# Kernel optimization log

Measured on AMD Instinct MI355X. Metric: run time of the kernel, lower is better.

## Reference

```python
import jax, jax.numpy as jnp
import numpy as np

B, CIN, HID, T, W, H, TAU = 8, 16, 64, 4, 32, 32, 5
EPS = 1e-5
DN = ('NCDHW', 'OIDHW', 'NCDHW')


def conv3d(x, w, b):
    # 'same' conv3d, NCDHW layout
    y = jax.lax.conv_general_dilated(x, w, (1, 1, 1), 'SAME', dimension_numbers=DN)
    return y + b[None, :, None, None, None]


def ln3(u):
    # F.layer_norm over the last 3 (spatial) dims, no affine
    mu = jnp.mean(u, axis=(-3, -2, -1), keepdims=True)
    var = jnp.var(u, axis=(-3, -2, -1), keepdims=True)
    return (u - mu) * jax.lax.rsqrt(var + EPS)


def ln4(u, w, b):
    # nn.LayerNorm(memory_shape): over last 4 dims (C,T,W,H), with affine
    mu = jnp.mean(u, axis=(-4, -3, -2, -1), keepdims=True)
    var = jnp.var(u, axis=(-4, -3, -2, -1), keepdims=True)
    return (u - mu) * jax.lax.rsqrt(var + EPS) * w + b


def self_attention(r, c_history):
    scale = 1.0 / np.sqrt(T * W * H)
    scores = jnp.einsum('bctwh,lbctwh->bl', r, c_history) * scale  # [B, TAU]
    # faithful to source: softmax over dim=0 (the batch axis of the [b,l] scores)
    attn = jax.nn.softmax(scores, axis=0)
    return jnp.einsum('bl,lbctwh->bctwh', attn, c_history)


def setup_inputs() -> dict:
    key = jax.random.key(0)
    ks = jax.random.split(key, 8)
    x = jax.random.normal(ks[0], (B, CIN, T, W, H), jnp.float32)
    c_history = jax.random.normal(ks[1], (TAU, B, HID, T, W, H), jnp.float32)
    m = jax.random.normal(ks[2], (B, HID, T, W, H), jnp.float32)
    h = jax.random.normal(ks[3], (B, HID, T, W, H), jnp.float32)
    Wx = jax.random.normal(ks[4], (7, HID, CIN, 3, 3, 3), jnp.float32) * 0.05
    bx = jnp.zeros((7, HID), jnp.float32)
    # 9 state-branch conv kernels: [hr, hi, hg, mi', mg', mf', ho, co, mo]
    Wh = jax.random.normal(ks[5], (9, HID, HID, 3, 3, 3), jnp.float32) * 0.02
    bh = jnp.zeros((9, HID), jnp.float32)
    w111 = jax.random.normal(ks[6], (HID, 2 * HID, 1, 1, 1), jnp.float32) * 0.05
    b111 = jnp.zeros((HID,), jnp.float32)
    ln_w = jnp.ones((HID, T, W, H), jnp.float32)
    ln_b = jnp.zeros((HID, T, W, H), jnp.float32)
    return dict(x=x, c_history=c_history, m=m, h=h, Wx=Wx, bx=bx, Wh=Wh, bh=bh,
                w111=w111, b111=b111, ln_w=ln_w, ln_b=ln_b)


def reference(x, c_history, m, h, Wx, bx, Wh, bh, w111, b111, ln_w, ln_b):
    cx = lambda i: conv3d(x, Wx[i], bx[i])
    cs = lambda u, i: conv3d(u, Wh[i], bh[i])
    r = jax.nn.sigmoid(ln3(cx(0) + cs(h, 0)))
    i = jax.nn.sigmoid(ln3(cx(1) + cs(h, 1)))
    g = jnp.tanh(ln3(cx(2) + cs(h, 2)))
    recall = self_attention(r, c_history)
    c = i * g + ln4(c_history[-1] + recall, ln_w, ln_b)
    i_p = jax.nn.sigmoid(ln3(cx(3) + cs(m, 3)))
    g_p = jnp.tanh(ln3(cx(4) + cs(m, 4)))
    f_p = jax.nn.sigmoid(ln3(cx(5) + cs(m, 5)))
    m_new = i_p * g_p + f_p * m
    o = jax.nn.sigmoid(ln3(cx(6) + cs(h, 6) + cs(c, 7) + cs(m_new, 8)))
    h_new = o * jnp.tanh(conv3d(jnp.concatenate([c, m_new], axis=1), w111, b111))
    c_history_new = jnp.concatenate([c_history[1:], c[None]], axis=0)
    return (c_history_new, m_new, h_new)
```

## Files before the change

kernel.cpp:

```cpp
#include <hip/hip_runtime.h>
#include <hip/hip_bf16.h>
#include <math.h>

#define BATCH 8
#define CIN 16
#define HID 64
#define S2 1024
#define SP 4096
#define CHB 262144
#define TAU 5
#define GATE_SZ 2097152
#define EPS 1e-5f

#define WS_Z_OFF   ((size_t)3 * GATE_SZ)
#define WS_ST_OFF  ((size_t)4 * GATE_SZ)

typedef unsigned short u16;
typedef __attribute__((ext_vector_type(8))) short  short8;
typedef __attribute__((ext_vector_type(8))) u16    ushort8;
typedef __attribute__((ext_vector_type(4))) float  f32x4;

#define N7 (7*27*64*96)
#define NO (27*64*128)
#define N1 (64*128)

__device__ __forceinline__ u16 f2b(float v) {
    __hip_bfloat16 h = __float2bfloat16(v);
    u16 r; __builtin_memcpy(&r, &h, 2); return r;
}

__device__ __forceinline__ float* gate_ptr(float* out, float* ws, int g) {
    return (g < 4) ? (out + (size_t)g * GATE_SZ) : (ws + (size_t)(g - 4) * GATE_SZ);
}

__global__ __launch_bounds__(256) void pack_w_k(const float* __restrict__ Wx,
                                                const float* __restrict__ Wh,
                                                const float* __restrict__ w111,
                                                u16* __restrict__ A7, u16* __restrict__ Ao,
                                                u16* __restrict__ A111)
{
    const int idx = blockIdx.x * 256 + threadIdx.x;
    if (idx < N7) {
        const int k = idx % 96, oc = (idx / 96) % 64, tap = (idx / (96*64)) % 27, g = idx / (96*64*27);
        float v = 0.f;
        if (k < 16)      v = Wx[((size_t)(g*64 + oc)*16 + k)      * 27 + tap];
        else if (k < 80) v = Wh[((size_t)(g*64 + oc)*64 + (k-16)) * 27 + tap];
        A7[idx] = f2b(v);
    } else if (idx < N7 + NO) {
        const int j = idx - N7;
        const int k = j % 128, oc = (j / 128) % 64, tap = j / (128*64);
        float v = (k < 64) ? Wh[((size_t)(7*64 + oc)*64 + k)      * 27 + tap]
                           : Wh[((size_t)(8*64 + oc)*64 + (k-64)) * 27 + tap];
        Ao[j] = f2b(v);
    } else if (idx < N7 + NO + N1) {
        const int j = idx - N7 - NO;
        A111[j] = f2b(w111[j]);
    }
}

__global__ __launch_bounds__(256) void pack_xhm_k(const float* __restrict__ x,
                                                  const float* __restrict__ h,
                                                  const float* __restrict__ m,
                                                  u16* __restrict__ XH, u16* __restrict__ XM)
{
    __shared__ float t[144][65];
    const int bi = blockIdx.x, b = bi >> 6, s0 = (bi & 63) << 6;
    for (int i = threadIdx.x; i < 144*64; i += 256) {
        const int row = i >> 6, sc = i & 63;
        float v;
        if (row < 16)      v = x[((size_t)b*16 + row)      * SP + s0 + sc];
        else if (row < 80) v = h[((size_t)b*64 + (row-16)) * SP + s0 + sc];
        else               v = m[((size_t)b*64 + (row-80)) * SP + s0 + sc];
        t[row][sc] = v;
    }
    __syncthreads();
    for (int j = threadIdx.x; j < 64*96; j += 256) {
        const int s = j / 96, ch = j % 96;
        const size_t o = ((size_t)b*4096 + s0 + s) * 96 + ch;
        XH[o] = f2b(ch < 80 ? t[ch][s] : 0.f);
        XM[o] = f2b(ch < 16 ? t[ch][s] : (ch < 80 ? t[ch + 64][s] : 0.f));
    }
}

template<int KCH, int TAPS, int NR, int MODE>
__global__ __launch_bounds__(256, 3) void conv_mfma_k(
    const u16* __restrict__ XA, const u16* __restrict__ XB,
    const u16* __restrict__ Apack,
    const float* __restrict__ bxp, const float* __restrict__ bhp,
    const float* __restrict__ b111,
    float* __restrict__ out, float* __restrict__ ws)
{
    constexpr int YT   = NR + 2;
    constexpr int ROWS = 4 * YT * 34;
    constexpr int PADK = 40;
    __shared__ __align__(16) u16 xs[ROWS * PADK];

    const int bi = blockIdx.x;
    int g = 0, b, y0, kh = 0, kc_lo = 0, kc_hi = KCH / 32;
    const u16* X; const u16* Ag; float* outp;
    if (MODE == 0) {
        constexpr int YB = 32 / NR;
        g  = bi / (8 * YB);
        b  = (bi / YB) % 8;
        y0 = (bi % YB) * NR;
        X  = (g >= 3 && g <= 5) ? XB : XA;
        Ag = Apack + (size_t)g * TAPS * 64 * KCH;
        outp = gate_ptr(out, ws, g) + (size_t)b * CHB;
    } else if (MODE == 1) {
        kh = bi >> 8; b = (bi >> 5) & 7; y0 = bi & 31;
        kc_lo = kh * 2; kc_hi = kc_lo + 2;
        X = XA; Ag = Apack;
        outp = ws + (size_t)2 * GATE_SZ + (size_t)b * CHB;
    } else {
        b = bi >> 5; y0 = bi & 31;
        X = XA; Ag = Apack;
        outp = ws + (size_t)b * CHB;
    }
    const u16* Xb = X + (size_t)b * 4096 * KCH;

    const int tid  = threadIdx.x;
    const int w    = tid >> 6;
    const int lane = tid & 63;
    const int xn   = lane & 15, quad = lane >> 4;

    f32x4 acc[4][2 * NR] = {};

    for (int kc = kc_lo; kc < kc_hi; ++kc) {
        if (kc != kc_lo) __syncthreads();
        for (int cix = tid; cix < ROWS * 4; cix += 256) {
            const int r = cix >> 2, sub = cix & 3;
            const int t = r / (YT * 34), rem = r % (YT * 34);
            const int yy = rem / 34, xx = rem % 34;
            const int gy = y0 + yy - 1, gx = xx - 1;
            ushort8 v = {0, 0, 0, 0, 0, 0, 0, 0};
            if ((unsigned)gy < 32u && (unsigned)gx < 32u)
                v = *(const ushort8*)&Xb[(size_t)(t * 1024 + gy * 32 + gx) * KCH + kc * 32 + sub * 8];
            *(ushort8*)&xs[r * PADK + sub * 8] = v;
        }
        __syncthreads();

        auto load_a = [&](short8* a, int tap) {
            #pragma unroll
            for (int mt = 0; mt < 4; ++mt)
                a[mt] = *(const short8*)&Ag[(size_t)(tap * 64 + mt * 16 + xn) * KCH + kc * 32 + quad * 8];
        };
        auto load_b = [&](short8* bf, int tap) {
            int kd, ky, kx;
            if (TAPS == 27) { kd = tap / 9; ky = (tap / 3) % 3; kx = tap % 3; }
            else            { kd = 1; ky = 1; kx = 1; }
            const int tin = w + kd - 1;
            #pragma unroll
            for (int nt = 0; nt < 2 * NR; ++nt) {
                const int ysub = nt >> 1, xh = nt & 1;
                bf[nt] = *(const short8*)
                    &xs[((tin * YT + ysub + ky) * 34 + xh * 16 + xn + kx) * PADK + quad * 8];
            }
        };
        auto do_mfma = [&](short8* a, short8* bf) {
            #pragma unroll
            for (int nt = 0; nt < 2 * NR; ++nt)
                #pragma unroll
                for (int mt = 0; mt < 4; ++mt)
                    acc[mt][nt] = __builtin_amdgcn_mfma_f32_16x16x32_bf16(a[mt], bf[nt], acc[mt][nt], 0, 0, 0);
        };

        if (TAPS == 27) {
            const int tap_lo = (w == 0) ? 9 : 0;
            const int tap_hi = (w == 3) ? 18 : 27;
            short8 a0[4], b0[2 * NR], a1[4], b1[2 * NR];
            load_a(a0, tap_lo); load_b(b0, tap_lo);
            int tap = tap_lo;
            for (; tap + 2 <= tap_hi; tap += 2) {
                load_a(a1, tap + 1); load_b(b1, tap + 1);
                do_mfma(a0, b0);
                if (tap + 2 < tap_hi) { load_a(a0, tap + 2); load_b(b0, tap + 2); }
                do_mfma(a1, b1);
            }
            if (tap < tap_hi) do_mfma(a0, b0);
        } else {
            short8 a0[4], b0[2 * NR];
            load_a(a0, 0); load_b(b0, 0);
            do_mfma(a0, b0);
        }
    }

    #pragma unroll
    for (int mt = 0; mt < 4; ++mt)
    #pragma unroll
    for (int nt = 0; nt < 2 * NR; ++nt) {
        const int ysub = nt >> 1, xh = nt & 1;
        const int sp = w * 1024 + (y0 + ysub) * 32 + xh * 16 + xn;
        #pragma unroll
        for (int reg = 0; reg < 4; ++reg) {
            const int oc = mt * 16 + quad * 4 + reg;
            float bias;
            if (MODE == 0)      bias = bxp[g * 64 + oc] + bhp[g * 64 + oc];
            else if (MODE == 1) bias = (kh == 0) ? (bhp[7 * 64 + oc] + bhp[8 * 64 + oc]) : 0.f;
            else                bias = b111[oc];
            const float vv = acc[mt][nt][reg] + bias;
            float* p = outp + (size_t)oc * SP + sp;
            if (MODE == 1) atomicAdd(p, vv); else *p = vv;
        }
    }
}

__global__ __launch_bounds__(256) void ln3_act_k(float* __restrict__ out,
                                                 float* __restrict__ ws, int gate0)
{
    const int blk = blockIdx.x;
    const int g = gate0 + (blk >> 9);
    float* p = gate_ptr(out, ws, g) + (size_t)(blk & 511) * SP;
    const int tid = threadIdx.x;

    float s = 0.f, s2 = 0.f;
    for (int k = tid; k < SP; k += 256) { float v = p[k]; s += v; s2 += v * v; }
    #pragma unroll
    for (int off = 32; off > 0; off >>= 1) { s += __shfl_down(s, off); s2 += __shfl_down(s2, off); }
    __shared__ float rs[4], rs2[4], stat[2];
    if ((tid & 63) == 0) { rs[tid >> 6] = s; rs2[tid >> 6] = s2; }
    __syncthreads();
    if (tid == 0) {
        float S  = rs[0] + rs[1] + rs[2] + rs[3];
        float Sq = rs2[0] + rs2[1] + rs2[2] + rs2[3];
        float mu  = S * (1.f / SP);
        float var = Sq * (1.f / SP) - mu * mu;
        stat[0] = mu; stat[1] = rsqrtf(var + EPS);
    }
    __syncthreads();
    const float mu = stat[0], r = stat[1];
    const bool use_tanh = (g == 2 || g == 4);
    for (int k = tid; k < SP; k += 256) {
        float v = (p[k] - mu) * r;
        p[k] = use_tanh ? tanhf(v) : 1.f / (1.f + expf(-v));
    }
}

__global__ __launch_bounds__(256) void scores_k(const float* __restrict__ r,
                                                const float* __restrict__ chist,
                                                float* __restrict__ stats)
{
    const int blk = blockIdx.x;
    const int chunk = blk & 7;
    const int bl = blk >> 3;
    const int l = bl % 5, b = bl / 5;
    const float* rp = r + (size_t)b * CHB;
    const float* cp = chist + (size_t)(l * BATCH + b) * CHB;
    float s = 0.f;
    const int lo = chunk * (CHB / 8);
    for (int k = lo + threadIdx.x; k < lo + CHB / 8; k += 256) s += rp[k] * cp[k];
    #pragma unroll
    for (int off = 32; off > 0; off >>= 1) s += __shfl_down(s, off);
    __shared__ float rsh[4];
    if ((threadIdx.x & 63) == 0) rsh[threadIdx.x >> 6] = s;
    __syncthreads();
    if (threadIdx.x == 0)
        atomicAdd(&stats[l * 8 + b], (rsh[0] + rsh[1] + rsh[2] + rsh[3]) * (1.f / 64.f));
}

__global__ void softmax_k(float* __restrict__ stats)
{
    int l = threadIdx.x;
    if (l < TAU) {
        float mx = -1e30f;
        for (int b = 0; b < BATCH; ++b) mx = fmaxf(mx, stats[l * 8 + b]);
        float e[BATCH]; float sum = 0.f;
        for (int b = 0; b < BATCH; ++b) { e[b] = expf(stats[l * 8 + b] - mx); sum += e[b]; }
        for (int b = 0; b < BATCH; ++b) stats[40 + l * 8 + b] = e[b] / sum;
    }
}

__global__ __launch_bounds__(256) void recall_k(const float* __restrict__ chist,
                                                float* __restrict__ ws,
                                                float* __restrict__ part)
{
    const float* stats = ws + WS_ST_OFF;
    const int blk = blockIdx.x;
    const int b = blk >> 10;
    const int idx = (blk & 1023) * 256 + threadIdx.x;
    const float a0 = stats[40 +  0 + b], a1 = stats[40 +  8 + b], a2 = stats[40 + 16 + b];
    const float a3 = stats[40 + 24 + b], a4 = stats[40 + 32 + b];
    const size_t e = (size_t)b * CHB + idx;
    const size_t LB = (size_t)BATCH * CHB;
    float z = chist[4 * LB + e] * (1.f + a4)
            + a0 * chist[0 * LB + e] + a1 * chist[1 * LB + e]
            + a2 * chist[2 * LB + e] + a3 * chist[3 * LB + e];
    ws[WS_Z_OFF + e] = z;

    float s = z, s2 = z * z;
    #pragma unroll
    for (int off = 32; off > 0; off >>= 1) { s += __shfl_down(s, off); s2 += __shfl_down(s2, off); }
    __shared__ float rs[4], rs2[4];
    if ((threadIdx.x & 63) == 0) { rs[threadIdx.x >> 6] = s; rs2[threadIdx.x >> 6] = s2; }
    __syncthreads();
    if (threadIdx.x == 0) {
        part[blk]        = rs[0] + rs[1] + rs[2] + rs[3];
        part[8192 + blk] = rs2[0] + rs2[1] + rs2[2] + rs2[3];
    }
}

__global__ __launch_bounds__(256) void ln4_stats_k(const float* __restrict__ part,
                                                   float* __restrict__ stats)
{
    const int b = blockIdx.x;
    float s = 0.f, s2 = 0.f;
    for (int j = threadIdx.x; j < 1024; j += 256) {
        s  += part[b * 1024 + j];
        s2 += part[8192 + b * 1024 + j];
    }
    #pragma unroll
    for (int off = 32; off > 0; off >>= 1) { s += __shfl_down(s, off); s2 += __shfl_down(s2, off); }
    __shared__ float rs[4], rs2[4];
    if ((threadIdx.x & 63) == 0) { rs[threadIdx.x >> 6] = s; rs2[threadIdx.x >> 6] = s2; }
    __syncthreads();
    if (threadIdx.x == 0) {
        float S  = rs[0] + rs[1] + rs[2] + rs[3];
        float Sq = rs2[0] + rs2[1] + rs2[2] + rs2[3];
        float mu  = S * (1.f / CHB);
        float var = Sq * (1.f / CHB) - mu * mu;
        stats[80 + b] = mu;
        stats[88 + b] = rsqrtf(var + EPS);
    }
}

__global__ __launch_bounds__(256) void cm_pcm_k(float* __restrict__ out, float* __restrict__ ws,
                                                const float* __restrict__ m,
                                                const float* __restrict__ lnw,
                                                const float* __restrict__ lnb,
                                                u16* __restrict__ PCM)
{
    __shared__ __align__(16) u16 tl[64][136];
    const int bi = blockIdx.x;
    const int b = bi >> 6;
    const int s0 = (bi & 63) << 6;
    const float* stats = ws + WS_ST_OFF;
    const float mu = stats[80 + b], rstd = stats[88 + b];

    for (int i = threadIdx.x; i < 1024; i += 256) {
        const int chn = i >> 4;
        const int sp4 = (i & 15) << 2;
        const size_t e = (size_t)b * CHB + (size_t)chn * SP + s0 + sp4;
        const size_t le = (size_t)chn * SP + s0 + sp4;
        float4 z  = *(const float4*)&ws[WS_Z_OFF + e];
        float4 gi = *(const float4*)&gate_ptr(out, ws, 1)[e];
        float4 gg = *(const float4*)&gate_ptr(out, ws, 2)[e];
        float4 ip = *(const float4*)&gate_ptr(out, ws, 3)[e];
        float4 gp = *(const float4*)&gate_ptr(out, ws, 4)[e];
        float4 fp = *(const float4*)&gate_ptr(out, ws, 5)[e];
        float4 mm = *(const float4*)&m[e];
        float4 lw = *(const float4*)&lnw[le];
        float4 lb = *(const float4*)&lnb[le];
        float4 c, mn;
        c.x = gi.x * gg.x + (z.x - mu) * rstd * lw.x + lb.x;
        c.y = gi.y * gg.y + (z.y - mu) * rstd * lw.y + lb.y;
        c.z = gi.z * gg.z + (z.z - mu) * rstd * lw.z + lb.z;
        c.w = gi.w * gg.w + (z.w - mu) * rstd * lw.w + lb.w;
        mn.x = ip.x * gp.x + fp.x * mm.x;
        mn.y = ip.y * gp.y + fp.y * mm.y;
        mn.z = ip.z * gp.z + fp.z * mm.z;
        mn.w = ip.w * gp.w + fp.w * mm.w;
        *(float4*)&out[(size_t)4 * GATE_SZ + e] = c;
        *(float4*)&out[(size_t)5 * GATE_SZ + e] = mn;
        const float cc[4] = {c.x, c.y, c.z, c.w};
        const float mm2[4] = {mn.x, mn.y, mn.z, mn.w};
        #pragma unroll
        for (int k = 0; k < 4; ++k) {
            tl[sp4 + k][chn]      = f2b(cc[k]);
            tl[sp4 + k][64 + chn] = f2b(mm2[k]);
        }
    }
    __syncthreads();
    for (int j = threadIdx.x; j < 1024; j += 256) {
        const int s = j >> 4, c8 = (j & 15) << 3;
        ushort8 v = *(const ushort8*)&tl[s][c8];
        *(ushort8*)&PCM[((size_t)b * 4096 + s0 + s) * 128 + c8] = v;
    }
}

__global__ __launch_bounds__(256) void hnew_elem_k(const float* __restrict__ o,
                                                   const float* __restrict__ v,
                                                   float* __restrict__ hn)
{
    const size_t i = (size_t)blockIdx.x * 256 + threadIdx.x;
    float4 ov = ((const float4*)o)[i], vv = ((const float4*)v)[i];
    float4 r;
    r.x = ov.x * tanhf(vv.x); r.y = ov.y * tanhf(vv.y);
    r.z = ov.z * tanhf(vv.z); r.w = ov.w * tanhf(vv.w);
    ((float4*)hn)[i] = r;
}

__global__ __launch_bounds__(256) void hist_copy_k(const float* __restrict__ chist,
                                                   float* __restrict__ out)
{
    const size_t i = (size_t)blockIdx.x * 256 + threadIdx.x;
    const float4* src = (const float4*)(chist + GATE_SZ);
    float4* dst = (float4*)out;
    dst[i] = src[i];
}

extern "C" void kernel_launch(void* const* d_in, const int* in_sizes, int n_in,
                              void* d_out, int out_size, void* d_ws, size_t ws_size,
                              hipStream_t stream)
{
    const float* x    = (const float*)d_in[0];
    const float* ch   = (const float*)d_in[1];
    const float* m    = (const float*)d_in[2];
    const float* h    = (const float*)d_in[3];
    const float* Wx   = (const float*)d_in[4];
    const float* bx   = (const float*)d_in[5];
    const float* Wh   = (const float*)d_in[6];
    const float* bh   = (const float*)d_in[7];
    const float* w111 = (const float*)d_in[8];
    const float* b111 = (const float*)d_in[9];
    const float* lnw  = (const float*)d_in[10];
    const float* lnb  = (const float*)d_in[11];
    float* out = (float*)d_out;
    float* ws  = (float*)d_ws;

    u16* XH   = (u16*)(out + (size_t)4 * GATE_SZ);
    u16* A7   = (u16*)(out + (size_t)5 * GATE_SZ);
    u16* XM   = (u16*)(out + (size_t)6 * GATE_SZ);
    u16* Ao   = XM + (size_t)BATCH * 4096 * 96;
    u16* A111 = Ao + (size_t)NO;
    u16* PCM  = (u16*)out;
    float* part  = out + (size_t)4 * GATE_SZ;
    float* stats = ws + WS_ST_OFF;

    hipMemsetAsync(stats, 0, 128 * sizeof(float), stream);
    pack_w_k<<<(N7 + NO + N1 + 255) / 256, 256, 0, stream>>>(Wx, Wh, w111, A7, Ao, A111);
    pack_xhm_k<<<512, 256, 0, stream>>>(x, h, m, XH, XM);

    conv_mfma_k<96, 27, 2, 0><<<896, 256, 0, stream>>>(XH, XM, A7, bx, bh, nullptr, out, ws);
    ln3_act_k<<<3072, 256, 0, stream>>>(out, ws, 0);

    scores_k<<<BATCH * TAU * 8, 256, 0, stream>>>(out, ch, stats);
    softmax_k<<<1, 64, 0, stream>>>(stats);
    recall_k<<<8192, 256, 0, stream>>>(ch, ws, part);
    ln4_stats_k<<<8, 256, 0, stream>>>(part, stats);
    cm_pcm_k<<<512, 256, 0, stream>>>(out, ws, m, lnw, lnb, PCM);

    conv_mfma_k<128, 27, 1, 1><<<512, 256, 0, stream>>>(PCM, nullptr, Ao, nullptr, bh, nullptr, out, ws);
    ln3_act_k<<<512, 256, 0, stream>>>(out, ws, 6);
    conv_mfma_k<128, 1, 1, 2><<<256, 256, 0, stream>>>(PCM, nullptr, A111, nullptr, nullptr, b111, out, ws);

    hnew_elem_k<<<GATE_SZ / 1024, 256, 0, stream>>>(ws + (size_t)2 * GATE_SZ, ws, out + (size_t)6 * GATE_SZ);
    hist_copy_k<<<8192, 256, 0, stream>>>(ch, out);
}
```

Before: 438.5 us.

## Swizzle conv LDS tile, raise occupancy, and fuse small attention/LN4/tail kernels

The conv kernel's shared-memory input tile drops its padding in favour of an XOR swizzle, which shrinks LDS use, and the occupancy hint goes from 3 to 4 blocks per CU. The scores kernel now reads r once per element for all five history steps. The softmax is folded into recall_k, the LN4 statistics into cm_pcm_k, the stats memset into pack_w_k, and hnew plus the history copy into one tail kernel. These changes cut launch count and repeated loads, at the cost of redundant per-block softmax and LN4-stat computation and possible register pressure at the higher occupancy target.

```diff
diff --git a/kernel.cpp b/kernel.cpp
--- a/kernel.cpp
+++ b/kernel.cpp
@@ -37,8 +37,10 @@
                                                 const float* __restrict__ Wh,
                                                 const float* __restrict__ w111,
                                                 u16* __restrict__ A7, u16* __restrict__ Ao,
-                                                u16* __restrict__ A111)
-{
+                                                u16* __restrict__ A111,
+                                                float* __restrict__ stats)
+{
+    if (blockIdx.x == 0 && threadIdx.x < 128) stats[threadIdx.x] = 0.f;
     const int idx = blockIdx.x * 256 + threadIdx.x;
     if (idx < N7) {
         const int k = idx % 96, oc = (idx / 96) % 64, tap = (idx / (96*64)) % 27, g = idx / (96*64*27);
@@ -82,8 +84,12 @@
     }
 }
 
+__device__ __forceinline__ int swz32(int r, int c) {
+    return r * 32 + ((c ^ ((r >> 1) & 3)) << 3);
+}
+
 template<int KCH, int TAPS, int NR, int MODE>
-__global__ __launch_bounds__(256, 3) void conv_mfma_k(
+__global__ __launch_bounds__(256, 4) void conv_mfma_k(
     const u16* __restrict__ XA, const u16* __restrict__ XB,
     const u16* __restrict__ Apack,
     const float* __restrict__ bxp, const float* __restrict__ bhp,
@@ -92,7 +98,7 @@
 {
     constexpr int YT   = NR + 2;
     constexpr int ROWS = 4 * YT * 34;
-    constexpr int PADK = 40;
+    constexpr int PADK = 32;
     __shared__ __align__(16) u16 xs[ROWS * PADK];
 
     const int bi = blockIdx.x;
@@ -135,7 +141,7 @@
             ushort8 v = {0, 0, 0, 0, 0, 0, 0, 0};
             if ((unsigned)gy < 32u && (unsigned)gx < 32u)
                 v = *(const ushort8*)&Xb[(size_t)(t * 1024 + gy * 32 + gx) * KCH + kc * 32 + sub * 8];
-            *(ushort8*)&xs[r * PADK + sub * 8] = v;
+            *(ushort8*)&xs[swz32(r, sub)] = v;
         }
         __syncthreads();
 
@@ -152,8 +158,8 @@
             #pragma unroll
             for (int nt = 0; nt < 2 * NR; ++nt) {
                 const int ysub = nt >> 1, xh = nt & 1;
-                bf[nt] = *(const short8*)
-                    &xs[((tin * YT + ysub + ky) * 34 + xh * 16 + xn + kx) * PADK + quad * 8];
+                const int row = (tin * YT + ysub + ky) * 34 + xh * 16 + xn + kx;
+                bf[nt] = *(const short8*)&xs[swz32(row, quad)];
             }
         };
         auto do_mfma = [&](short8* a, short8* bf) {
@@ -240,32 +246,28 @@
                                                 float* __restrict__ stats)
 {
     const int blk = blockIdx.x;
-    const int chunk = blk & 7;
-    const int bl = blk >> 3;
-    const int l = bl % 5, b = bl / 5;
+    const int b = blk >> 6, chunk = blk & 63;
     const float* rp = r + (size_t)b * CHB;
-    const float* cp = chist + (size_t)(l * BATCH + b) * CHB;
-    float s = 0.f;
-    const int lo = chunk * (CHB / 8);
-    for (int k = lo + threadIdx.x; k < lo + CHB / 8; k += 256) s += rp[k] * cp[k];
-    #pragma unroll
-    for (int off = 32; off > 0; off >>= 1) s += __shfl_down(s, off);
-    __shared__ float rsh[4];
-    if ((threadIdx.x & 63) == 0) rsh[threadIdx.x >> 6] = s;
-    __syncthreads();
-    if (threadIdx.x == 0)
-        atomicAdd(&stats[l * 8 + b], (rsh[0] + rsh[1] + rsh[2] + rsh[3]) * (1.f / 64.f));
-}
-
-__global__ void softmax_k(float* __restrict__ stats)
-{
-    int l = threadIdx.x;
-    if (l < TAU) {
-        float mx = -1e30f;
-        for (int b = 0; b < BATCH; ++b) mx = fmaxf(mx, stats[l * 8 + b]);
-        float e[BATCH]; float sum = 0.f;
-        for (int b = 0; b < BATCH; ++b) { e[b] = expf(stats[l * 8 + b] - mx); sum += e[b]; }
-        for (int b = 0; b < BATCH; ++b) stats[40 + l * 8 + b] = e[b] / sum;
+    const int lo = chunk * (CHB / 64);
+    float s[TAU] = {};
+    for (int k = lo + threadIdx.x; k < lo + CHB / 64; k += 256) {
+        const float rv = rp[k];
+        #pragma unroll
+        for (int l = 0; l < TAU; ++l) s[l] += rv * chist[(size_t)(l * BATCH + b) * CHB + k];
+    }
+    __shared__ float rsh[TAU][4];
+    #pragma unroll
+    for (int l = 0; l < TAU; ++l) {
+        float v = s[l];
+        #pragma unroll
+        for (int off = 32; off > 0; off >>= 1) v += __shfl_down(v, off);
+        if ((threadIdx.x & 63) == 0) rsh[l][threadIdx.x >> 6] = v;
+    }
+    __syncthreads();
+    if (threadIdx.x < TAU) {
+        const int l = threadIdx.x;
+        atomicAdd(&stats[l * 8 + b],
+                  (rsh[l][0] + rsh[l][1] + rsh[l][2] + rsh[l][3]) * (1.f / 64.f));
     }
 }
 
@@ -277,8 +279,23 @@
     const int blk = blockIdx.x;
     const int b = blk >> 10;
     const int idx = (blk & 1023) * 256 + threadIdx.x;
-    const float a0 = stats[40 +  0 + b], a1 = stats[40 +  8 + b], a2 = stats[40 + 16 + b];
-    const float a3 = stats[40 + 24 + b], a4 = stats[40 + 32 + b];
+
+    __shared__ float attn[TAU];
+    if (threadIdx.x < TAU) {
+        const int l = threadIdx.x;
+        float mx = -1e30f;
+        for (int bb = 0; bb < BATCH; ++bb) mx = fmaxf(mx, stats[l * 8 + bb]);
+        float sum = 0.f, e = 0.f;
+        for (int bb = 0; bb < BATCH; ++bb) {
+            float t = expf(stats[l * 8 + bb] - mx);
+            sum += t;
+            if (bb == b) e = t;
+        }
+        attn[l] = e / sum;
+    }
+    __syncthreads();
+    const float a0 = attn[0], a1 = attn[1], a2 = attn[2], a3 = attn[3], a4 = attn[4];
+
     const size_t e = (size_t)b * CHB + idx;
     const size_t LB = (size_t)BATCH * CHB;
     float z = chist[4 * LB + e] * (1.f + a4)
@@ -298,10 +315,18 @@
     }
 }
 
-__global__ __launch_bounds__(256) void ln4_stats_k(const float* __restrict__ part,
-                                                   float* __restrict__ stats)
-{
-    const int b = blockIdx.x;
+__global__ __launch_bounds__(256) void cm_pcm_k(float* __restrict__ out, float* __restrict__ ws,
+                                                const float* __restrict__ m,
+                                                const float* __restrict__ lnw,
+                                                const float* __restrict__ lnb,
+                                                const float* __restrict__ part,
+                                                u16* __restrict__ PCM)
+{
+    __shared__ __align__(16) u16 tl[64][136];
+    const int bi = blockIdx.x;
+    const int b = bi >> 6;
+    const int s0 = (bi & 63) << 6;
+
     float s = 0.f, s2 = 0.f;
     for (int j = threadIdx.x; j < 1024; j += 256) {
         s  += part[b * 1024 + j];
@@ -309,7 +334,7 @@
     }
     #pragma unroll
     for (int off = 32; off > 0; off >>= 1) { s += __shfl_down(s, off); s2 += __shfl_down(s2, off); }
-    __shared__ float rs[4], rs2[4];
+    __shared__ float rs[4], rs2[4], st[2];
     if ((threadIdx.x & 63) == 0) { rs[threadIdx.x >> 6] = s; rs2[threadIdx.x >> 6] = s2; }
     __syncthreads();
     if (threadIdx.x == 0) {
@@ -317,23 +342,10 @@
         float Sq = rs2[0] + rs2[1] + rs2[2] + rs2[3];
         float mu  = S * (1.f / CHB);
         float var = Sq * (1.f / CHB) - mu * mu;
-        stats[80 + b] = mu;
-        stats[88 + b] = rsqrtf(var + EPS);
-    }
-}
-
-__global__ __launch_bounds__(256) void cm_pcm_k(float* __restrict__ out, float* __restrict__ ws,
-                                                const float* __restrict__ m,
-                                                const float* __restrict__ lnw,
-                                                const float* __restrict__ lnb,
-                                                u16* __restrict__ PCM)
-{
-    __shared__ __align__(16) u16 tl[64][136];
-    const int bi = blockIdx.x;
-    const int b = bi >> 6;
-    const int s0 = (bi & 63) << 6;
-    const float* stats = ws + WS_ST_OFF;
-    const float mu = stats[80 + b], rstd = stats[88 + b];
+        st[0] = mu; st[1] = rsqrtf(var + EPS);
+    }
+    __syncthreads();
+    const float mu = st[0], rstd = st[1];
 
     for (int i = threadIdx.x; i < 1024; i += 256) {
         const int chn = i >> 4;
@@ -370,31 +382,29 @@
     }
     __syncthreads();
     for (int j = threadIdx.x; j < 1024; j += 256) {
-        const int s = j >> 4, c8 = (j & 15) << 3;
-        ushort8 v = *(const ushort8*)&tl[s][c8];
-        *(ushort8*)&PCM[((size_t)b * 4096 + s0 + s) * 128 + c8] = v;
-    }
-}
-
-__global__ __launch_bounds__(256) void hnew_elem_k(const float* __restrict__ o,
-                                                   const float* __restrict__ v,
-                                                   float* __restrict__ hn)
-{
-    const size_t i = (size_t)blockIdx.x * 256 + threadIdx.x;
-    float4 ov = ((const float4*)o)[i], vv = ((const float4*)v)[i];
-    float4 r;
-    r.x = ov.x * tanhf(vv.x); r.y = ov.y * tanhf(vv.y);
-    r.z = ov.z * tanhf(vv.z); r.w = ov.w * tanhf(vv.w);
-    ((float4*)hn)[i] = r;
-}
-
-__global__ __launch_bounds__(256) void hist_copy_k(const float* __restrict__ chist,
-                                                   float* __restrict__ out)
-{
-    const size_t i = (size_t)blockIdx.x * 256 + threadIdx.x;
-    const float4* src = (const float4*)(chist + GATE_SZ);
-    float4* dst = (float4*)out;
-    dst[i] = src[i];
+        const int sidx = j >> 4, c8 = (j & 15) << 3;
+        ushort8 v = *(const ushort8*)&tl[sidx][c8];
+        *(ushort8*)&PCM[((size_t)b * 4096 + s0 + sidx) * 128 + c8] = v;
+    }
+}
+
+__global__ __launch_bounds__(256) void tail_k(const float* __restrict__ chist,
+                                              const float* __restrict__ o,
+                                              const float* __restrict__ v,
+                                              float* __restrict__ out)
+{
+    const int bi = blockIdx.x;
+    if (bi < 8192) {
+        const size_t i = (size_t)bi * 256 + threadIdx.x;
+        ((float4*)out)[i] = ((const float4*)(chist + GATE_SZ))[i];
+    } else {
+        const size_t i = (size_t)(bi - 8192) * 256 + threadIdx.x;
+        float4 ov = ((const float4*)o)[i], vv = ((const float4*)v)[i];
+        float4 r;
+        r.x = ov.x * tanhf(vv.x); r.y = ov.y * tanhf(vv.y);
+        r.z = ov.z * tanhf(vv.z); r.w = ov.w * tanhf(vv.w);
+        ((float4*)(out + (size_t)6 * GATE_SZ))[i] = r;
+    }
 }
 
 extern "C" void kernel_launch(void* const* d_in, const int* in_sizes, int n_in,
@@ -422,26 +432,22 @@
     u16* Ao   = XM + (size_t)BATCH * 4096 * 96;
     u16* A111 = Ao + (size_t)NO;
     u16* PCM  = (u16*)out;
-    float* part  = out + (size_t)4 * GATE_SZ;
+    float* part  = (float*)(A111 + N1);
     float* stats = ws + WS_ST_OFF;
 
-    hipMemsetAsync(stats, 0, 128 * sizeof(float), stream);
-    pack_w_k<<<(N7 + NO + N1 + 255) / 256, 256, 0, stream>>>(Wx, Wh, w111, A7, Ao, A111);
+    pack_w_k<<<(N7 + NO + N1 + 255) / 256, 256, 0, stream>>>(Wx, Wh, w111, A7, Ao, A111, stats);
     pack_xhm_k<<<512, 256, 0, stream>>>(x, h, m, XH, XM);
 
     conv_mfma_k<96, 27, 2, 0><<<896, 256, 0, stream>>>(XH, XM, A7, bx, bh, nullptr, out, ws);
     ln3_act_k<<<3072, 256, 0, stream>>>(out, ws, 0);
 
-    scores_k<<<BATCH * TAU * 8, 256, 0, stream>>>(out, ch, stats);
-    softmax_k<<<1, 64, 0, stream>>>(stats);
+    scores_k<<<512, 256, 0, stream>>>(out, ch, stats);
     recall_k<<<8192, 256, 0, stream>>>(ch, ws, part);
-    ln4_stats_k<<<8, 256, 0, stream>>>(part, stats);
-    cm_pcm_k<<<512, 256, 0, stream>>>(out, ws, m, lnw, lnb, PCM);
+    cm_pcm_k<<<512, 256, 0, stream>>>(out, ws, m, lnw, lnb, part, PCM);
 
     conv_mfma_k<128, 27, 1, 1><<<512, 256, 0, stream>>>(PCM, nullptr, Ao, nullptr, bh, nullptr, out, ws);
     ln3_act_k<<<512, 256, 0, stream>>>(out, ws, 6);
     conv_mfma_k<128, 1, 1, 2><<<256, 256, 0, stream>>>(PCM, nullptr, A111, nullptr, nullptr, b111, out, ws);
 
-    hnew_elem_k<<<GATE_SZ / 1024, 256, 0, stream>>>(ws + (size_t)2 * GATE_SZ, ws, out + (size_t)6 * GATE_SZ);
-    hist_copy_k<<<8192, 256, 0, stream>>>(ch, out);
-}
+    tail_k<<<10240, 256, 0, stream>>>(ch, ws + (size_t)2 * GATE_SZ, ws, out);
+}
```

Result: slower. 553.7 us (+26.3%).
